# Kernel optimization log

Hardware: AMD Instinct MI355X
Metric: run time of the kernel (lower is better)

## Reference

```python
import jax, jax.numpy as jnp
import numpy as np
from jax import lax

THR = 1.0
BETA = 0.9
SLOPE = 25.0  # fast_sigmoid surrogate slope
N_JOINTS = 6

@jax.custom_vjp
def spike_fn(x):
    # Heaviside forward, fast_sigmoid surrogate backward (snntorch surrogate.fast_sigmoid)
    return (x > 0).astype(x.dtype)

def _spike_fwd(x):
    return spike_fn(x), x

def _spike_bwd(x, g):
    return (g / (SLOPE * jnp.abs(x) + 1.0) ** 2,)

spike_fn.defvjp(_spike_fwd, _spike_bwd)

def lif(cur, mem):
    # snntorch Leaky, reset_mechanism='subtract': reset from previous mem (detached)
    reset = lax.stop_gradient(spike_fn(mem - THR))
    mem = BETA * mem + cur - reset * THR
    spk = spike_fn(mem - THR)
    return spk, mem

def rate_encode(data, u):
    # data: (B, F), u: (T, B, F) uniform[0,1) -> binary spikes (T, B, F)
    dmin = jnp.min(data, axis=1, keepdims=True)
    dmax = jnp.max(data, axis=1, keepdims=True)
    rng = dmax - dmin
    rng = jnp.where(rng == 0, jnp.ones_like(rng), rng)
    norm = (data - dmin) / rng
    prob = jnp.clip(100.0 * norm * 0.001, 0.0, 1.0)  # max_rate=100, dt=0.001
    return (u < prob[None]).astype(jnp.float32)

def conv1x1(x, W, b):
    # x: (B, Cin, H, 1), W: (Cout, Cin, 1, 1)
    y = lax.conv_general_dilated(x, W, (1, 1), 'VALID',
                                 dimension_numbers=('NCHW', 'OIHW', 'NCHW'))
    return y + b[None, :, None, None]

def setup_inputs() -> dict:
    key = jax.random.key(0)
    ks = jax.random.split(key, 16)
    B, T, n = 8192, 200, N_JOINTS
    inp = {
        'x':  jax.random.normal(ks[0], (B, 3 * n), jnp.float32),
        'u1': jax.random.uniform(ks[1], (T, B, 2 * n), jnp.float32),
        'u2': jax.random.uniform(ks[2], (T, B, n), jnp.float32),
        'u3': jax.random.uniform(ks[3], (T, B, n), jnp.float32),
        'W1': jax.random.normal(ks[4], (256, 12), jnp.float32) * 0.2,
        'b1': jax.random.normal(ks[5], (256,), jnp.float32) * 0.05,
        'W2': jax.random.normal(ks[6], (256, 256), jnp.float32) * 0.06,
        'b2': jax.random.normal(ks[7], (256,), jnp.float32) * 0.05,
        'W3': jax.random.normal(ks[8], (6, 256), jnp.float32) * 0.06,
        'b3': jax.random.normal(ks[9], (6,), jnp.float32) * 0.05,
        'Wc1': jax.random.normal(ks[10], (32, 3, 1, 1), jnp.float32) * 0.5,
        'bc1': jax.random.normal(ks[11], (32,), jnp.float32) * 0.05,
        'Wc2': jax.random.normal(ks[12], (64, 32, 1, 1), jnp.float32) * 0.15,
        'bc2': jax.random.normal(ks[13], (64,), jnp.float32) * 0.05,
        'WA': jax.random.normal(ks[14], (1, 64), jnp.float32) * 0.12,
    }
    return inp

def reference(x, u1, u2, u3, W1, b1, W2, b2, W3, b3, Wc1, bc1, Wc2, bc2, WA):
    n = N_JOINTS
    B = x.shape[0]
    spk_in = rate_encode(x[:, :2 * n], u1)        # (T, B, 2n)
    spk_thdot = rate_encode(x[:, n:2 * n], u2)    # (T, B, n)
    spk_thdot2 = rate_encode(x[:, 2 * n:], u3)    # (T, B, n)

    mem1 = jnp.zeros((B, 256), jnp.float32)
    mem2 = jnp.zeros((B, 256), jnp.float32)
    mem3 = jnp.zeros((B, n), jnp.float32)
    mem4 = jnp.zeros((B, 32, n, 1), jnp.float32)
    conv_out0 = jnp.zeros((B, 64, n, 1), jnp.float32)

    def step(carry, inp):
        m1, m2, m3, m4, _ = carry
        s_in, s_td, s_td2 = inp
        spk1, m1 = lif(s_in @ W1.T + b1, m1)
        spk2, m2 = lif(spk1 @ W2.T + b2, m2)
        spk3, m3 = lif(spk2 @ W3.T + b3, m3)
        spk_conv = jnp.stack([s_td, spk3, s_td2], axis=1)[..., None]  # (B,3,n,1)
        cur4 = conv1x1(spk_conv, Wc1, bc1)  # maxpool1 with k=1 is identity
        spk4, m4 = lif(cur4, m4)
        conv_out = conv1x1(spk4, Wc2, bc2)  # maxpool2 with k=1 is identity
        return (m1, m2, m3, m4, conv_out), None

    (_, _, _, _, conv_out), _ = lax.scan(step, (mem1, mem2, mem3, mem4, conv_out0),
                                         (spk_in, spk_thdot, spk_thdot2))
    # c.T: out_a/b/c = fc_A(conv_out[:, :, i, 0]) for i in 0..2, no bias
    c_t = jnp.einsum('bcm,c->bm', conv_out[:, :, :3, 0], WA[0])  # (B, 3)
    return c_t
```

## Files before the change

### kernel.cpp

```cpp
#include <hip/hip_runtime.h>
#include <cstdint>
#include <cstddef>

typedef unsigned long long u64;

__global__ void prep_weights(const float* __restrict__ W2, const float* __restrict__ Wc2,
                             const float* __restrict__ bc2, const float* __restrict__ WA,
                             float* __restrict__ Wt2f, double* __restrict__ wEff,
                             double* __restrict__ bEff)
{
  int id = blockIdx.x * 256 + (int)threadIdx.x;
  if (id < 65536){ int i = id >> 8, j = id & 255; Wt2f[(i<<8)+j] = W2[j*256+i]; }
  else if (id < 65792){ Wt2f[id] = 0.0f; }
  if (id < 32){ double s = 0.0; for (int c=0;c<64;c++) s += (double)WA[c]*(double)Wc2[c*32+id]; wEff[id] = s; }
  if (id == 32){ double s = 0.0; for (int c=0;c<64;c++) s += (double)WA[c]*(double)bc2[c]; *bEff = s; }
}

__global__ void prep_probs(const float* __restrict__ x, double* __restrict__ probs, int B)
{
  int b = blockIdx.x, k = (int)threadIdx.x;
  if (b >= B || k >= 24) return;
  double* pb = probs + (size_t)b*24;
  if (k >= 18){ pb[k] = -1.0; return; }
  int fk, g0, gn;
  if (k < 12){ fk = k;          g0 = 0;  gn = 12; }
  else if (k < 15){ fk = 6+(k-12);  g0 = 6;  gn = 6; }
  else           { fk = 12+(k-15); g0 = 12; gn = 6; }
  const float* xb = x + (size_t)b*18;
  double mn = (double)xb[g0], mx = mn;
  for (int f = 1; f < gn; f++){ double v = (double)xb[g0+f]; mn = fmin(mn, v); mx = fmax(mx, v); }
  double rng = mx - mn; if (rng == 0.0) rng = 1.0;
  double norm = ((double)xb[fk] - mn) / rng;
  double p = (100.0 * norm) * 0.001;
  p = fmin(fmax(p, 0.0), 1.0);
  pb[k] = p;
}

__global__ void prep_enc(const float* __restrict__ u1, const float* __restrict__ u2,
                         const float* __restrict__ u3, const double* __restrict__ probs,
                         unsigned* __restrict__ encT, int B, int T)
{
  int b = blockIdx.x * blockDim.x + (int)threadIdx.x;
  int t = blockIdx.y;
  if (b >= B) return;
  if (t >= T){ encT[(size_t)b*(T+2) + t] = 0u; return; }
  const double* pb = probs + (size_t)b*24;
  size_t r = (size_t)t * B + b;
  const float* a1 = u1 + r*12;
  const float* a2 = u2 + r*6;
  const float* a3 = u3 + r*6;
  unsigned e = 0;
  #pragma unroll
  for (int k = 0; k < 12; k++) if ((double)a1[k] < pb[k])    e |= (1u << k);
  #pragma unroll
  for (int h = 0; h < 3; h++)  if ((double)a2[h] < pb[12+h]) e |= (1u << (12+h));
  #pragma unroll
  for (int h = 0; h < 3; h++)  if ((double)a3[h] < pb[15+h]) e |= (1u << (15+h));
  encT[(size_t)b*(T+2) + t] = e;
}

__global__ __launch_bounds__(256) void snn_main(
    const unsigned* __restrict__ encT,
    const float* __restrict__ b1, const float* __restrict__ b2, const float* __restrict__ b3,
    const float* __restrict__ W1, const float* __restrict__ W3,
    const float* __restrict__ Wc1, const float* __restrict__ bc1,
    const float* __restrict__ Wt2f,
    const double* __restrict__ wEff, const double* __restrict__ bEff,
    float* __restrict__ out, int B, int T)
{
  __shared__ __align__(16) float s_w1[12*256];
  __shared__ __align__(16) float s_w3[257*4];

  const int tid  = (int)threadIdx.x;
  const int lane = tid & 63;
  const int wid  = tid >> 6;
  const int b = blockIdx.x * 4 + wid;
  const int l4 = lane << 2;
  const int lcl = (lane < 3) ? lane : 3;

  for (int i = tid; i < 3072; i += 256){ int k = i >> 8, j = i & 255; s_w1[i] = W1[j*12+k]; }
  for (int i = tid; i < 1028; i += 256){
    int r = i >> 2, c = i & 3;
    s_w3[i] = (r < 256 && c < 3) ? W3[c*256 + r] : 0.0f;
  }
  __syncthreads();
  if (b >= B) return;

  const float4 b1f = *(const float4*)(b1 + l4);
  const float4 b2f = *(const float4*)(b2 + l4);
  const double b1d0=b1f.x, b1d1=b1f.y, b1d2=b1f.z, b1d3=b1f.w;
  const double b2d0=b2f.x, b2d1=b2f.y, b2d2=b2f.z, b2d3=b2f.w;
  const double b3d = (lane < 3) ? (double)b3[lane] : 0.0;
  double wc1b=0.0, wEd=0.0, pre0=0.0, pre1=0.0, pre2=0.0, pre3=0.0;
  if (lane < 32){
    double wa = (double)Wc1[lane*3+0];
    wc1b      = (double)Wc1[lane*3+1];
    double wc = (double)Wc1[lane*3+2];
    double bd = (double)bc1[lane];
    wEd  = wEff[lane];
    pre0 = bd;
    pre1 = bd + wa;
    pre2 = bd + wc;
    pre3 = bd + wa + wc;
  }

  double m10=0,m11=0,m12=0,m13=0;
  double m20=0,m21=0,m22=0,m23=0;
  double m3v=0;
  double m40=0,m41=0,m42=0;
  bool sp20=false,sp21=false,sp22=false,sp23=false;
  bool sp3v=false;
  bool sp40=false,sp41=false,sp42=false;

  const unsigned* encTb = encT + (size_t)b * (T + 2);

  unsigned e_cur = __builtin_amdgcn_readfirstlane(encTb[0]);
  unsigned e_nx  = __builtin_amdgcn_readfirstlane(encTb[1]);
  double ca0=b1d0, ca1=b1d1, ca2=b1d2, ca3=b1d3;
  {
    unsigned w = e_cur & 0xFFFu;
    while (w){
      int k = __builtin_ctz(w); w &= w-1;
      const float4 r = *(const float4*)&s_w1[(k<<8) + l4];
      ca0 += (double)r.x; ca1 += (double)r.y; ca2 += (double)r.z; ca3 += (double)r.w;
    }
  }

  for (int t = 0; t < T; t++){
    m10 = fma(0.9, m10, ca0);
    m11 = fma(0.9, m11, ca1);
    m12 = fma(0.9, m12, ca2);
    m13 = fma(0.9, m13, ca3);
    const bool sp10 = m10 > 1.0; u64 w0 = __ballot(sp10);
    const bool sp11 = m11 > 1.0; u64 w1 = __ballot(sp11);
    const bool sp12 = m12 > 1.0; u64 w2 = __ballot(sp12);
    const bool sp13 = m13 > 1.0; u64 w3m = __ballot(sp13);

    int i0 = w0  ? (((int)__builtin_ctzll(w0) <<2)|0) : 256;  w0  &= w0 -1;
    int i1 = w1  ? (((int)__builtin_ctzll(w1) <<2)|1) : 256;  w1  &= w1 -1;
    int i2 = w2  ? (((int)__builtin_ctzll(w2) <<2)|2) : 256;  w2  &= w2 -1;
    int i3 = w3m ? (((int)__builtin_ctzll(w3m)<<2)|3) : 256;  w3m &= w3m-1;
    const float4 r0 = *(const float4*)(Wt2f + ((size_t)i0<<8) + l4);
    const float4 r1 = *(const float4*)(Wt2f + ((size_t)i1<<8) + l4);
    const float4 r2 = *(const float4*)(Wt2f + ((size_t)i2<<8) + l4);
    const float4 r3 = *(const float4*)(Wt2f + ((size_t)i3<<8) + l4);

    const unsigned e_n2 = encTb[t+2];

    ca0 = (sp10 ? -1.0 : 0.0) + b1d0;
    ca1 = (sp11 ? -1.0 : 0.0) + b1d1;
    ca2 = (sp12 ? -1.0 : 0.0) + b1d2;
    ca3 = (sp13 ? -1.0 : 0.0) + b1d3;
    {
      unsigned w = e_nx & 0xFFFu;
      while (w){
        int k = __builtin_ctz(w); w &= w-1;
        const float4 r = *(const float4*)&s_w1[(k<<8) + l4];
        ca0 += (double)r.x; ca1 += (double)r.y; ca2 += (double)r.z; ca3 += (double)r.w;
      }
    }

    double c0 = (sp20 ? -1.0 : 0.0) + b2d0;
    double c1 = (sp21 ? -1.0 : 0.0) + b2d1;
    double c2 = (sp22 ? -1.0 : 0.0) + b2d2;
    double c3 = (sp23 ? -1.0 : 0.0) + b2d3;
    c0 += (double)r0.x; c1 += (double)r0.y; c2 += (double)r0.z; c3 += (double)r0.w;
    c0 += (double)r1.x; c1 += (double)r1.y; c2 += (double)r1.z; c3 += (double)r1.w;
    c0 += (double)r2.x; c1 += (double)r2.y; c2 += (double)r2.z; c3 += (double)r2.w;
    c0 += (double)r3.x; c1 += (double)r3.y; c2 += (double)r3.z; c3 += (double)r3.w;

    while (w0 | w1 | w2 | w3m){
      int j0 = w0  ? (((int)__builtin_ctzll(w0) <<2)|0) : 256;  w0  &= w0 -1;
      int j1 = w1  ? (((int)__builtin_ctzll(w1) <<2)|1) : 256;  w1  &= w1 -1;
      int j2 = w2  ? (((int)__builtin_ctzll(w2) <<2)|2) : 256;  w2  &= w2 -1;
      int j3 = w3m ? (((int)__builtin_ctzll(w3m)<<2)|3) : 256;  w3m &= w3m-1;
      const float4 q0 = *(const float4*)(Wt2f + ((size_t)j0<<8) + l4);
      const float4 q1 = *(const float4*)(Wt2f + ((size_t)j1<<8) + l4);
      const float4 q2 = *(const float4*)(Wt2f + ((size_t)j2<<8) + l4);
      const float4 q3 = *(const float4*)(Wt2f + ((size_t)j3<<8) + l4);
      c0 += (double)q0.x; c1 += (double)q0.y; c2 += (double)q0.z; c3 += (double)q0.w;
      c0 += (double)q1.x; c1 += (double)q1.y; c2 += (double)q1.z; c3 += (double)q1.w;
      c0 += (double)q2.x; c1 += (double)q2.y; c2 += (double)q2.z; c3 += (double)q2.w;
      c0 += (double)q3.x; c1 += (double)q3.y; c2 += (double)q3.z; c3 += (double)q3.w;
    }

    m20 = fma(0.9, m20, c0);
    m21 = fma(0.9, m21, c1);
    m22 = fma(0.9, m22, c2);
    m23 = fma(0.9, m23, c3);
    sp20 = m20 > 1.0; u64 v0 = __ballot(sp20);
    sp21 = m21 > 1.0; u64 v1 = __ballot(sp21);
    sp22 = m22 > 1.0; u64 v2 = __ballot(sp22);
    sp23 = m23 > 1.0; u64 v3 = __ballot(sp23);

    double cl3 = (sp3v ? -1.0 : 0.0) + b3d;
    while (v0 | v1 | v2 | v3){
      int j0 = v0 ? (((int)__builtin_ctzll(v0)<<2)|0) : 256;  v0 &= v0-1;
      int j1 = v1 ? (((int)__builtin_ctzll(v1)<<2)|1) : 256;  v1 &= v1-1;
      int j2 = v2 ? (((int)__builtin_ctzll(v2)<<2)|2) : 256;  v2 &= v2-1;
      int j3 = v3 ? (((int)__builtin_ctzll(v3)<<2)|3) : 256;  v3 &= v3-1;
      cl3 += (double)s_w3[(j0<<2) + lcl];
      cl3 += (double)s_w3[(j1<<2) + lcl];
      cl3 += (double)s_w3[(j2<<2) + lcl];
      cl3 += (double)s_w3[(j3<<2) + lcl];
    }
    m3v = fma(0.9, m3v, cl3);
    sp3v = m3v > 1.0;
    const unsigned s3 = (unsigned)(__ballot((lane < 3) && sp3v) & 7ull);

    const unsigned td  = (e_cur >> 12) & 7u;
    const unsigned td2 = (e_cur >> 15) & 7u;
    {
      double cur, t1, t2;
      t1 = (td2 & 1u) ? pre2 : pre0;  t2 = (td2 & 1u) ? pre3 : pre1;
      cur = (td & 1u) ? t2 : t1;
      if (s3 & 1u) cur += wc1b;
      cur += sp40 ? -1.0 : 0.0;
      m40 = fma(0.9, m40, cur); sp40 = m40 > 1.0;
      t1 = (td2 & 2u) ? pre2 : pre0;  t2 = (td2 & 2u) ? pre3 : pre1;
      cur = (td & 2u) ? t2 : t1;
      if (s3 & 2u) cur += wc1b;
      cur += sp41 ? -1.0 : 0.0;
      m41 = fma(0.9, m41, cur); sp41 = m41 > 1.0;
      t1 = (td2 & 4u) ? pre2 : pre0;  t2 = (td2 & 4u) ? pre3 : pre1;
      cur = (td & 4u) ? t2 : t1;
      if (s3 & 4u) cur += wc1b;
      cur += sp42 ? -1.0 : 0.0;
      m42 = fma(0.9, m42, cur); sp42 = m42 > 1.0;
    }

    e_cur = e_nx;
    e_nx  = __builtin_amdgcn_readfirstlane(e_n2);
  }

  double o0 = sp40 ? wEd : 0.0;
  double o1 = sp41 ? wEd : 0.0;
  double o2 = sp42 ? wEd : 0.0;
  for (int off = 32; off > 0; off >>= 1){
    o0 += __shfl_xor(o0, off, 64);
    o1 += __shfl_xor(o1, off, 64);
    o2 += __shfl_xor(o2, off, 64);
  }
  if (lane == 0){
    const double be = *bEff;
    out[b*3+0] = (float)(o0 + be);
    out[b*3+1] = (float)(o1 + be);
    out[b*3+2] = (float)(o2 + be);
  }
}

extern "C" void kernel_launch(void* const* d_in, const int* in_sizes, int n_in,
                              void* d_out, int out_size, void* d_ws, size_t ws_size,
                              hipStream_t stream)
{
  const float* x   = (const float*)d_in[0];
  const float* u1  = (const float*)d_in[1];
  const float* u2  = (const float*)d_in[2];
  const float* u3  = (const float*)d_in[3];
  const float* W1  = (const float*)d_in[4];
  const float* b1  = (const float*)d_in[5];
  const float* W2  = (const float*)d_in[6];
  const float* b2  = (const float*)d_in[7];
  const float* W3  = (const float*)d_in[8];
  const float* b3  = (const float*)d_in[9];
  const float* Wc1 = (const float*)d_in[10];
  const float* bc1 = (const float*)d_in[11];
  const float* Wc2 = (const float*)d_in[12];
  const float* bc2 = (const float*)d_in[13];
  const float* WA  = (const float*)d_in[14];
  float* out = (float*)d_out;

  const int B = in_sizes[0] / 18;
  const int T = in_sizes[1] / (B * 12);

  char* ws = (char*)d_ws;
  float*  Wt2f  = (float*)(ws + 0);
  double* wEff  = (double*)(ws + 263168);
  double* bEff  = (double*)(ws + 263424);
  double* probs = (double*)(ws + 263432);
  unsigned* encT= (unsigned*)(ws + 263432 + (size_t)B*24*8);

  hipLaunchKernelGGL(prep_weights, dim3(257), dim3(256), 0, stream,
                     W2, Wc2, bc2, WA, Wt2f, wEff, bEff);
  hipLaunchKernelGGL(prep_probs, dim3(B), dim3(64), 0, stream, x, probs, B);
  hipLaunchKernelGGL(prep_enc, dim3((B+255)/256, T+2), dim3(256), 0, stream,
                     u1, u2, u3, probs, encT, B, T);
  hipLaunchKernelGGL(snn_main, dim3((B+3)/4), dim3(256), 0, stream,
                     encT, b1, b2, b3, W1, W3, Wc1, bc1, Wt2f, wEff, bEff, out, B, T);
}
```

Before: 717.1 us.

## Stage half of W2 in LDS, 1024-thread blocks with two rows per wave

The main kernel now copies the first 128 rows of the transposed W2 (about 129 KB) into shared memory and sums layer-2 contributions from those rows via LDS, while the other 128 rows are still gathered from global memory. Blocks grow to 1024 threads and each wave handles two batch rows back to back, so the LDS copy is shared across 32 rows. The layer-1 input accumulation is unrolled four at a time using a zero padding row. The intent is to cut global and L2 gather traffic for the sparse W2 row sums, at the cost of a large LDS footprint that allows only one block per CU and more register pressure from the doubled per-wave state.

Result: slower. 881.1 us (+22.9%).

```diff
diff --git a/kernel.cpp b/kernel.cpp
--- a/kernel.cpp
+++ b/kernel.cpp
@@ -59,7 +59,7 @@
   encT[(size_t)b*(T+2) + t] = e;
 }
 
-__global__ __launch_bounds__(256) void snn_main(
+__global__ __launch_bounds__(1024, 4) void snn_main(
     const unsigned* __restrict__ encT,
     const float* __restrict__ b1, const float* __restrict__ b2, const float* __restrict__ b3,
     const float* __restrict__ W1, const float* __restrict__ W3,
@@ -68,184 +68,215 @@
     const double* __restrict__ wEff, const double* __restrict__ bEff,
     float* __restrict__ out, int B, int T)
 {
-  __shared__ __align__(16) float s_w1[12*256];
+  __shared__ __align__(16) float s_w2[129*256];
+  __shared__ __align__(16) float s_w1[13*256];
   __shared__ __align__(16) float s_w3[257*4];
 
   const int tid  = (int)threadIdx.x;
   const int lane = tid & 63;
-  const int wid  = tid >> 6;
-  const int b = blockIdx.x * 4 + wid;
-  const int l4 = lane << 2;
-  const int lcl = (lane < 3) ? lane : 3;
-
-  for (int i = tid; i < 3072; i += 256){ int k = i >> 8, j = i & 255; s_w1[i] = W1[j*12+k]; }
-  for (int i = tid; i < 1028; i += 256){
+  const int wv   = tid >> 6;
+  const int l4   = lane << 2;
+  const int lcl  = (lane < 3) ? lane : 3;
+
+  {
+    const float4* src = (const float4*)Wt2f;
+    float4* dst = (float4*)s_w2;
+    #pragma unroll
+    for (int i = 0; i < 8; i++) dst[tid + (i << 10)] = src[tid + (i << 10)];
+    if (tid < 64) dst[8192 + tid] = make_float4(0.f, 0.f, 0.f, 0.f);
+  }
+  for (int i = tid; i < 13*256; i += 1024){
+    int k = i >> 8, j = i & 255;
+    s_w1[i] = (k < 12) ? W1[j*12 + k] : 0.f;
+  }
+  for (int i = tid; i < 1028; i += 1024){
     int r = i >> 2, c = i & 3;
-    s_w3[i] = (r < 256 && c < 3) ? W3[c*256 + r] : 0.0f;
+    s_w3[i] = (r < 256 && c < 3) ? W3[c*256 + r] : 0.f;
   }
   __syncthreads();
-  if (b >= B) return;
+
+  const int r0 = blockIdx.x * 32 + wv * 2;
 
   const float4 b1f = *(const float4*)(b1 + l4);
   const float4 b2f = *(const float4*)(b2 + l4);
   const double b1d0=b1f.x, b1d1=b1f.y, b1d2=b1f.z, b1d3=b1f.w;
   const double b2d0=b2f.x, b2d1=b2f.y, b2d2=b2f.z, b2d3=b2f.w;
-  const double b3d = (lane < 3) ? (double)b3[lane] : 0.0;
-  double wc1b=0.0, wEd=0.0, pre0=0.0, pre1=0.0, pre2=0.0, pre3=0.0;
+  const float  b3f = (lane < 3) ? b3[lane] : 0.f;
+  double wc1b=0.0, pre0=0.0, pre1=0.0, pre2=0.0, pre3=0.0;
   if (lane < 32){
     double wa = (double)Wc1[lane*3+0];
     wc1b      = (double)Wc1[lane*3+1];
     double wc = (double)Wc1[lane*3+2];
     double bd = (double)bc1[lane];
-    wEd  = wEff[lane];
     pre0 = bd;
     pre1 = bd + wa;
     pre2 = bd + wc;
     pre3 = bd + wa + wc;
   }
 
-  double m10=0,m11=0,m12=0,m13=0;
-  double m20=0,m21=0,m22=0,m23=0;
-  double m3v=0;
-  double m40=0,m41=0,m42=0;
-  bool sp20=false,sp21=false,sp22=false,sp23=false;
-  bool sp3v=false;
-  bool sp40=false,sp41=false,sp42=false;
-
-  const unsigned* encTb = encT + (size_t)b * (T + 2);
-
-  unsigned e_cur = __builtin_amdgcn_readfirstlane(encTb[0]);
-  unsigned e_nx  = __builtin_amdgcn_readfirstlane(encTb[1]);
-  double ca0=b1d0, ca1=b1d1, ca2=b1d2, ca3=b1d3;
-  {
-    unsigned w = e_cur & 0xFFFu;
-    while (w){
-      int k = __builtin_ctz(w); w &= w-1;
-      const float4 r = *(const float4*)&s_w1[(k<<8) + l4];
-      ca0 += (double)r.x; ca1 += (double)r.y; ca2 += (double)r.z; ca3 += (double)r.w;
+  double m1[2][4] = {}, m2[2][4] = {}, m3[2] = {}, m4[2][3] = {};
+
+  const unsigned* ebp[2];
+  ebp[0] = encT + (size_t)((r0     < B) ? r0     : 0) * (T + 2);
+  ebp[1] = encT + (size_t)((r0 + 1 < B) ? r0 + 1 : 0) * (T + 2);
+  unsigned ecur[2], enx[2];
+  #pragma unroll
+  for (int rr = 0; rr < 2; rr++){
+    ecur[rr] = __builtin_amdgcn_readfirstlane(ebp[rr][0]);
+    enx[rr]  = __builtin_amdgcn_readfirstlane(ebp[rr][1]);
+  }
+
+  for (int t = 0; t < T; t++){
+    #pragma unroll
+    for (int rr = 0; rr < 2; rr++){
+      double a0 = ((m1[rr][0] > 1.0) ? -1.0 : 0.0) + b1d0;
+      double a1 = ((m1[rr][1] > 1.0) ? -1.0 : 0.0) + b1d1;
+      double a2 = ((m1[rr][2] > 1.0) ? -1.0 : 0.0) + b1d2;
+      double a3 = ((m1[rr][3] > 1.0) ? -1.0 : 0.0) + b1d3;
+      {
+        unsigned w = ecur[rr] & 0xFFFu;
+        while (w){
+          int k0 = __builtin_ctz(w); w &= w-1;
+          int k1 = 12, k2 = 12, k3 = 12;
+          if (w){ k1 = __builtin_ctz(w); w &= w-1;
+            if (w){ k2 = __builtin_ctz(w); w &= w-1;
+              if (w){ k3 = __builtin_ctz(w); w &= w-1; } } }
+          const float4 qa = *(const float4*)&s_w1[(k0<<8)+l4];
+          const float4 qb = *(const float4*)&s_w1[(k1<<8)+l4];
+          const float4 qc = *(const float4*)&s_w1[(k2<<8)+l4];
+          const float4 qd = *(const float4*)&s_w1[(k3<<8)+l4];
+          a0 += (double)qa.x; a1 += (double)qa.y; a2 += (double)qa.z; a3 += (double)qa.w;
+          a0 += (double)qb.x; a1 += (double)qb.y; a2 += (double)qb.z; a3 += (double)qb.w;
+          a0 += (double)qc.x; a1 += (double)qc.y; a2 += (double)qc.z; a3 += (double)qc.w;
+          a0 += (double)qd.x; a1 += (double)qd.y; a2 += (double)qd.z; a3 += (double)qd.w;
+        }
+      }
+      m1[rr][0] = fma(0.9, m1[rr][0], a0);
+      m1[rr][1] = fma(0.9, m1[rr][1], a1);
+      m1[rr][2] = fma(0.9, m1[rr][2], a2);
+      m1[rr][3] = fma(0.9, m1[rr][3], a3);
+      u64 w0 = __ballot(m1[rr][0] > 1.0);
+      u64 w1 = __ballot(m1[rr][1] > 1.0);
+      u64 w2 = __ballot(m1[rr][2] > 1.0);
+      u64 w3m = __ballot(m1[rr][3] > 1.0);
+      u64 wl0 = w0 & 0xFFFFFFFFull, wg0 = w0 >> 32;
+      u64 wl1 = w1 & 0xFFFFFFFFull, wg1 = w1 >> 32;
+      u64 wl2 = w2 & 0xFFFFFFFFull, wg2 = w2 >> 32;
+      u64 wl3 = w3m & 0xFFFFFFFFull, wg3 = w3m >> 32;
+
+      int i0 = wg0 ? (((int)__builtin_ctzll(wg0)<<2)|0)+128 : 256;  wg0 &= wg0-1;
+      int i1 = wg1 ? (((int)__builtin_ctzll(wg1)<<2)|1)+128 : 256;  wg1 &= wg1-1;
+      int i2 = wg2 ? (((int)__builtin_ctzll(wg2)<<2)|2)+128 : 256;  wg2 &= wg2-1;
+      int i3 = wg3 ? (((int)__builtin_ctzll(wg3)<<2)|3)+128 : 256;  wg3 &= wg3-1;
+      const float4 g0 = *(const float4*)(Wt2f + ((size_t)i0<<8) + l4);
+      const float4 g1 = *(const float4*)(Wt2f + ((size_t)i1<<8) + l4);
+      const float4 g2 = *(const float4*)(Wt2f + ((size_t)i2<<8) + l4);
+      const float4 g3 = *(const float4*)(Wt2f + ((size_t)i3<<8) + l4);
+
+      const unsigned e2 = ebp[rr][t+2];
+
+      double c0 = ((m2[rr][0] > 1.0) ? -1.0 : 0.0) + b2d0;
+      double c1 = ((m2[rr][1] > 1.0) ? -1.0 : 0.0) + b2d1;
+      double c2 = ((m2[rr][2] > 1.0) ? -1.0 : 0.0) + b2d2;
+      double c3 = ((m2[rr][3] > 1.0) ? -1.0 : 0.0) + b2d3;
+      while (wl0 | wl1 | wl2 | wl3){
+        int j0 = wl0 ? (((int)__builtin_ctzll(wl0)<<2)|0) : 128;  wl0 &= wl0-1;
+        int j1 = wl1 ? (((int)__builtin_ctzll(wl1)<<2)|1) : 128;  wl1 &= wl1-1;
+        int j2 = wl2 ? (((int)__builtin_ctzll(wl2)<<2)|2) : 128;  wl2 &= wl2-1;
+        int j3 = wl3 ? (((int)__builtin_ctzll(wl3)<<2)|3) : 128;  wl3 &= wl3-1;
+        const float4 q0 = *(const float4*)&s_w2[(j0<<8)+l4];
+        const float4 q1 = *(const float4*)&s_w2[(j1<<8)+l4];
+        const float4 q2 = *(const float4*)&s_w2[(j2<<8)+l4];
+        const float4 q3 = *(const float4*)&s_w2[(j3<<8)+l4];
+        c0 += (double)q0.x; c1 += (double)q0.y; c2 += (double)q0.z; c3 += (double)q0.w;
+        c0 += (double)q1.x; c1 += (double)q1.y; c2 += (double)q1.z; c3 += (double)q1.w;
+        c0 += (double)q2.x; c1 += (double)q2.y; c2 += (double)q2.z; c3 += (double)q2.w;
+        c0 += (double)q3.x; c1 += (double)q3.y; c2 += (double)q3.z; c3 += (double)q3.w;
+      }
+      c0 += (double)g0.x; c1 += (double)g0.y; c2 += (double)g0.z; c3 += (double)g0.w;
+      c0 += (double)g1.x; c1 += (double)g1.y; c2 += (double)g1.z; c3 += (double)g1.w;
+      c0 += (double)g2.x; c1 += (double)g2.y; c2 += (double)g2.z; c3 += (double)g2.w;
+      c0 += (double)g3.x; c1 += (double)g3.y; c2 += (double)g3.z; c3 += (double)g3.w;
+      while (wg0 | wg1 | wg2 | wg3){
+        int j0 = wg0 ? (((int)__builtin_ctzll(wg0)<<2)|0)+128 : 256;  wg0 &= wg0-1;
+        int j1 = wg1 ? (((int)__builtin_ctzll(wg1)<<2)|1)+128 : 256;  wg1 &= wg1-1;
+        int j2 = wg2 ? (((int)__builtin_ctzll(wg2)<<2)|2)+128 : 256;  wg2 &= wg2-1;
+        int j3 = wg3 ? (((int)__builtin_ctzll(wg3)<<2)|3)+128 : 256;  wg3 &= wg3-1;
+        const float4 h0 = *(const float4*)(Wt2f + ((size_t)j0<<8) + l4);
+        const float4 h1 = *(const float4*)(Wt2f + ((size_t)j1<<8) + l4);
+        const float4 h2 = *(const float4*)(Wt2f + ((size_t)j2<<8) + l4);
+        const float4 h3 = *(const float4*)(Wt2f + ((size_t)j3<<8) + l4);
+        c0 += (double)h0.x; c1 += (double)h0.y; c2 += (double)h0.z; c3 += (double)h0.w;
+        c0 += (double)h1.x; c1 += (double)h1.y; c2 += (double)h1.z; c3 += (double)h1.w;
+        c0 += (double)h2.x; c1 += (double)h2.y; c2 += (double)h2.z; c3 += (double)h2.w;
+        c0 += (double)h3.x; c1 += (double)h3.y; c2 += (double)h3.z; c3 += (double)h3.w;
+      }
+      m2[rr][0] = fma(0.9, m2[rr][0], c0);
+      m2[rr][1] = fma(0.9, m2[rr][1], c1);
+      m2[rr][2] = fma(0.9, m2[rr][2], c2);
+      m2[rr][3] = fma(0.9, m2[rr][3], c3);
+      u64 v0 = __ballot(m2[rr][0] > 1.0);
+      u64 v1 = __ballot(m2[rr][1] > 1.0);
+      u64 v2 = __ballot(m2[rr][2] > 1.0);
+      u64 v3 = __ballot(m2[rr][3] > 1.0);
+
+      double cl3 = ((m3[rr] > 1.0) ? -1.0 : 0.0) + (double)b3f;
+      while (v0 | v1 | v2 | v3){
+        int j0 = v0 ? (((int)__builtin_ctzll(v0)<<2)|0) : 256;  v0 &= v0-1;
+        int j1 = v1 ? (((int)__builtin_ctzll(v1)<<2)|1) : 256;  v1 &= v1-1;
+        int j2 = v2 ? (((int)__builtin_ctzll(v2)<<2)|2) : 256;  v2 &= v2-1;
+        int j3 = v3 ? (((int)__builtin_ctzll(v3)<<2)|3) : 256;  v3 &= v3-1;
+        cl3 += (double)s_w3[(j0<<2) + lcl];
+        cl3 += (double)s_w3[(j1<<2) + lcl];
+        cl3 += (double)s_w3[(j2<<2) + lcl];
+        cl3 += (double)s_w3[(j3<<2) + lcl];
+      }
+      m3[rr] = fma(0.9, m3[rr], cl3);
+      const unsigned s3 = (unsigned)(__ballot((lane < 3) && (m3[rr] > 1.0)) & 7ull);
+
+      const unsigned td  = (ecur[rr] >> 12) & 7u;
+      const unsigned td2 = (ecur[rr] >> 15) & 7u;
+      {
+        double cur, t1v, t2v;
+        t1v = (td2 & 1u) ? pre2 : pre0;  t2v = (td2 & 1u) ? pre3 : pre1;
+        cur = (td & 1u) ? t2v : t1v;
+        if (s3 & 1u) cur += wc1b;
+        cur += (m4[rr][0] > 1.0) ? -1.0 : 0.0;
+        m4[rr][0] = fma(0.9, m4[rr][0], cur);
+        t1v = (td2 & 2u) ? pre2 : pre0;  t2v = (td2 & 2u) ? pre3 : pre1;
+        cur = (td & 2u) ? t2v : t1v;
+        if (s3 & 2u) cur += wc1b;
+        cur += (m4[rr][1] > 1.0) ? -1.0 : 0.0;
+        m4[rr][1] = fma(0.9, m4[rr][1], cur);
+        t1v = (td2 & 4u) ? pre2 : pre0;  t2v = (td2 & 4u) ? pre3 : pre1;
+        cur = (td & 4u) ? t2v : t1v;
+        if (s3 & 4u) cur += wc1b;
+        cur += (m4[rr][2] > 1.0) ? -1.0 : 0.0;
+        m4[rr][2] = fma(0.9, m4[rr][2], cur);
+      }
+
+      ecur[rr] = enx[rr];
+      enx[rr]  = __builtin_amdgcn_readfirstlane(e2);
     }
   }
 
-  for (int t = 0; t < T; t++){
-    m10 = fma(0.9, m10, ca0);
-    m11 = fma(0.9, m11, ca1);
-    m12 = fma(0.9, m12, ca2);
-    m13 = fma(0.9, m13, ca3);
-    const bool sp10 = m10 > 1.0; u64 w0 = __ballot(sp10);
-    const bool sp11 = m11 > 1.0; u64 w1 = __ballot(sp11);
-    const bool sp12 = m12 > 1.0; u64 w2 = __ballot(sp12);
-    const bool sp13 = m13 > 1.0; u64 w3m = __ballot(sp13);
-
-    int i0 = w0  ? (((int)__builtin_ctzll(w0) <<2)|0) : 256;  w0  &= w0 -1;
-    int i1 = w1  ? (((int)__builtin_ctzll(w1) <<2)|1) : 256;  w1  &= w1 -1;
-    int i2 = w2  ? (((int)__builtin_ctzll(w2) <<2)|2) : 256;  w2  &= w2 -1;
-    int i3 = w3m ? (((int)__builtin_ctzll(w3m)<<2)|3) : 256;  w3m &= w3m-1;
-    const float4 r0 = *(const float4*)(Wt2f + ((size_t)i0<<8) + l4);
-    const float4 r1 = *(const float4*)(Wt2f + ((size_t)i1<<8) + l4);
-    const float4 r2 = *(const float4*)(Wt2f + ((size_t)i2<<8) + l4);
-    const float4 r3 = *(const float4*)(Wt2f + ((size_t)i3<<8) + l4);
-
-    const unsigned e_n2 = encTb[t+2];
-
-    ca0 = (sp10 ? -1.0 : 0.0) + b1d0;
-    ca1 = (sp11 ? -1.0 : 0.0) + b1d1;
-    ca2 = (sp12 ? -1.0 : 0.0) + b1d2;
-    ca3 = (sp13 ? -1.0 : 0.0) + b1d3;
-    {
-      unsigned w = e_nx & 0xFFFu;
-      while (w){
-        int k = __builtin_ctz(w); w &= w-1;
-        const float4 r = *(const float4*)&s_w1[(k<<8) + l4];
-        ca0 += (double)r.x; ca1 += (double)r.y; ca2 += (double)r.z; ca3 += (double)r.w;
-      }
+  const double wEd = (lane < 32) ? wEff[lane] : 0.0;
+  const double be = *bEff;
+  #pragma unroll
+  for (int rr = 0; rr < 2; rr++){
+    double o0 = ((lane < 32) && (m4[rr][0] > 1.0)) ? wEd : 0.0;
+    double o1 = ((lane < 32) && (m4[rr][1] > 1.0)) ? wEd : 0.0;
+    double o2 = ((lane < 32) && (m4[rr][2] > 1.0)) ? wEd : 0.0;
+    for (int off = 32; off > 0; off >>= 1){
+      o0 += __shfl_xor(o0, off, 64);
+      o1 += __shfl_xor(o1, off, 64);
+      o2 += __shfl_xor(o2, off, 64);
     }
-
-    double c0 = (sp20 ? -1.0 : 0.0) + b2d0;
-    double c1 = (sp21 ? -1.0 : 0.0) + b2d1;
-    double c2 = (sp22 ? -1.0 : 0.0) + b2d2;
-    double c3 = (sp23 ? -1.0 : 0.0) + b2d3;
-    c0 += (double)r0.x; c1 += (double)r0.y; c2 += (double)r0.z; c3 += (double)r0.w;
-    c0 += (double)r1.x; c1 += (double)r1.y; c2 += (double)r1.z; c3 += (double)r1.w;
-    c0 += (double)r2.x; c1 += (double)r2.y; c2 += (double)r2.z; c3 += (double)r2.w;
-    c0 += (double)r3.x; c1 += (double)r3.y; c2 += (double)r3.z; c3 += (double)r3.w;
-
-    while (w0 | w1 | w2 | w3m){
-      int j0 = w0  ? (((int)__builtin_ctzll(w0) <<2)|0) : 256;  w0  &= w0 -1;
-      int j1 = w1  ? (((int)__builtin_ctzll(w1) <<2)|1) : 256;  w1  &= w1 -1;
-      int j2 = w2  ? (((int)__builtin_ctzll(w2) <<2)|2) : 256;  w2  &= w2 -1;
-      int j3 = w3m ? (((int)__builtin_ctzll(w3m)<<2)|3) : 256;  w3m &= w3m-1;
-      const float4 q0 = *(const float4*)(Wt2f + ((size_t)j0<<8) + l4);
-      const float4 q1 = *(const float4*)(Wt2f + ((size_t)j1<<8) + l4);
-      const float4 q2 = *(const float4*)(Wt2f + ((size_t)j2<<8) + l4);
-      const float4 q3 = *(const float4*)(Wt2f + ((size_t)j3<<8) + l4);
-      c0 += (double)q0.x; c1 += (double)q0.y; c2 += (double)q0.z; c3 += (double)q0.w;
-      c0 += (double)q1.x; c1 += (double)q1.y; c2 += (double)q1.z; c3 += (double)q1.w;
-      c0 += (double)q2.x; c1 += (double)q2.y; c2 += (double)q2.z; c3 += (double)q2.w;
-      c0 += (double)q3.x; c1 += (double)q3.y; c2 += (double)q3.z; c3 += (double)q3.w;
+    if (lane == 0 && (r0 + rr) < B){
+      out[(r0+rr)*3+0] = (float)(o0 + be);
+      out[(r0+rr)*3+1] = (float)(o1 + be);
+      out[(r0+rr)*3+2] = (float)(o2 + be);
     }
-
-    m20 = fma(0.9, m20, c0);
-    m21 = fma(0.9, m21, c1);
-    m22 = fma(0.9, m22, c2);
-    m23 = fma(0.9, m23, c3);
-    sp20 = m20 > 1.0; u64 v0 = __ballot(sp20);
-    sp21 = m21 > 1.0; u64 v1 = __ballot(sp21);
-    sp22 = m22 > 1.0; u64 v2 = __ballot(sp22);
-    sp23 = m23 > 1.0; u64 v3 = __ballot(sp23);
-
-    double cl3 = (sp3v ? -1.0 : 0.0) + b3d;
-    while (v0 | v1 | v2 | v3){
-      int j0 = v0 ? (((int)__builtin_ctzll(v0)<<2)|0) : 256;  v0 &= v0-1;
-      int j1 = v1 ? (((int)__builtin_ctzll(v1)<<2)|1) : 256;  v1 &= v1-1;
-      int j2 = v2 ? (((int)__builtin_ctzll(v2)<<2)|2) : 256;  v2 &= v2-1;
-      int j3 = v3 ? (((int)__builtin_ctzll(v3)<<2)|3) : 256;  v3 &= v3-1;
-      cl3 += (double)s_w3[(j0<<2) + lcl];
-      cl3 += (double)s_w3[(j1<<2) + lcl];
-      cl3 += (double)s_w3[(j2<<2) + lcl];
-      cl3 += (double)s_w3[(j3<<2) + lcl];
-    }
-    m3v = fma(0.9, m3v, cl3);
-    sp3v = m3v > 1.0;
-    const unsigned s3 = (unsigned)(__ballot((lane < 3) && sp3v) & 7ull);
-
-    const unsigned td  = (e_cur >> 12) & 7u;
-    const unsigned td2 = (e_cur >> 15) & 7u;
-    {
-      double cur, t1, t2;
-      t1 = (td2 & 1u) ? pre2 : pre0;  t2 = (td2 & 1u) ? pre3 : pre1;
-      cur = (td & 1u) ? t2 : t1;
-      if (s3 & 1u) cur += wc1b;
-      cur += sp40 ? -1.0 : 0.0;
-      m40 = fma(0.9, m40, cur); sp40 = m40 > 1.0;
-      t1 = (td2 & 2u) ? pre2 : pre0;  t2 = (td2 & 2u) ? pre3 : pre1;
-      cur = (td & 2u) ? t2 : t1;
-      if (s3 & 2u) cur += wc1b;
-      cur += sp41 ? -1.0 : 0.0;
-      m41 = fma(0.9, m41, cur); sp41 = m41 > 1.0;
-      t1 = (td2 & 4u) ? pre2 : pre0;  t2 = (td2 & 4u) ? pre3 : pre1;
-      cur = (td & 4u) ? t2 : t1;
-      if (s3 & 4u) cur += wc1b;
-      cur += sp42 ? -1.0 : 0.0;
-      m42 = fma(0.9, m42, cur); sp42 = m42 > 1.0;
-    }
-
-    e_cur = e_nx;
-    e_nx  = __builtin_amdgcn_readfirstlane(e_n2);
-  }
-
-  double o0 = sp40 ? wEd : 0.0;
-  double o1 = sp41 ? wEd : 0.0;
-  double o2 = sp42 ? wEd : 0.0;
-  for (int off = 32; off > 0; off >>= 1){
-    o0 += __shfl_xor(o0, off, 64);
-    o1 += __shfl_xor(o1, off, 64);
-    o2 += __shfl_xor(o2, off, 64);
-  }
-  if (lane == 0){
-    const double be = *bEff;
-    out[b*3+0] = (float)(o0 + be);
-    out[b*3+1] = (float)(o1 + be);
-    out[b*3+2] = (float)(o2 + be);
   }
 }
 
@@ -285,6 +316,6 @@
   hipLaunchKernelGGL(prep_probs, dim3(B), dim3(64), 0, stream, x, probs, B);
   hipLaunchKernelGGL(prep_enc, dim3((B+255)/256, T+2), dim3(256), 0, stream,
                      u1, u2, u3, probs, encT, B, T);
-  hipLaunchKernelGGL(snn_main, dim3((B+3)/4), dim3(256), 0, stream,
+  hipLaunchKernelGGL(snn_main, dim3((B+31)/32), dim3(1024), 0, stream,
                      encT, b1, b2, b3, W1, W3, Wc1, bc1, Wt2f, wEff, bEff, out, B, T);
 }
```
